# Performance work log

Hardware: AMD Instinct MI355X
Metric: run time of the kernel (lower is better)

The kernel has to match this reference:

```python
import jax, jax.numpy as jnp
import numpy as np

BETA = 0.25


def setup_inputs() -> dict:
    key = jax.random.key(0)
    k1, = jax.random.split(key, 1)
    N, D, LEVELS = 1048576, 32, 8
    z_e = jax.random.normal(k1, (N, D), dtype=jnp.float32)
    grid = jnp.linspace(-1.0, 1.0, LEVELS, dtype=jnp.float32)  # FSQ buffer
    return {"z_e": z_e, "grid": grid}


def reference(z_e, grid):
    levels = grid.shape[0]  # static
    z_norm = jnp.tanh(z_e)                                   # [N, D]
    # nearest-level search over the tiny grid (faithful abs-distance argmin)
    dist = jnp.abs(z_norm[:, :, None] - grid[None, None, :])  # [N, D, L]
    indices = jnp.argmin(dist, axis=-1)                       # [N, D] int
    z_q = grid[indices]                                       # [N, D]

    codebook_loss = jnp.mean((z_q - jax.lax.stop_gradient(z_norm)) ** 2)
    commitment_loss = jnp.mean((z_norm - jax.lax.stop_gradient(z_q)) ** 2)
    loss = codebook_loss + BETA * commitment_loss

    # straight-through estimator
    z_q_st = z_norm + jax.lax.stop_gradient(z_q - z_norm)

    # mixed code over first <=4 dims, perplexity = unique fraction
    code_dims = min(indices.shape[1], 4)
    bases = (levels ** jnp.arange(code_dims)).astype(indices.dtype)  # [code_dims]
    mixed_indices = jnp.sum(indices[:, :code_dims] * bases[None, :], axis=1)  # [N]
    n_codes = levels ** code_dims  # static small (4096)
    occupancy = jnp.bincount(mixed_indices, length=n_codes) > 0
    unique_codes = jnp.sum(occupancy).astype(z_e.dtype)
    perplexity = unique_codes / jnp.asarray(float(max(mixed_indices.size, 1)), z_e.dtype)

    return z_q_st, mixed_indices, loss, perplexity
```

## Files before the change

### kernel.cpp

```cpp
#include <hip/hip_runtime.h>
#include <math.h>

#define DD 32
#define NB 2048
#define BS 256

typedef float f32x4 __attribute__((ext_vector_type(4)));

__device__ __forceinline__ unsigned int fkey(float f) {
    unsigned int u = __float_as_uint(f);
    return (u & 0x80000000u) ? ~u : (u | 0x80000000u);
}
__device__ __forceinline__ float funkey(unsigned int k) {
    unsigned int u = (k & 0x80000000u) ? (k ^ 0x80000000u) : ~k;
    return __uint_as_float(u);
}

__global__ __launch_bounds__(256) void fsq_main(
    const float* __restrict__ ze,
    const float* __restrict__ grid,
    float* __restrict__ out,
    int N,
    float* __restrict__ partials,
    int* __restrict__ occ)
{
    __shared__ float gs[8];
    __shared__ float ts[7];
    if (threadIdx.x < 8) gs[threadIdx.x] = grid[threadIdx.x];
    if (threadIdx.x < 7) {
        float a = grid[threadIdx.x], b = grid[threadIdx.x + 1];
        unsigned int lo = fkey(a), hi = fkey(b);
        while (hi - lo > 1u) {
            unsigned int mid = lo + (hi - lo) / 2u;
            float x = funkey(mid);
            if (fabsf(x - b) < fabsf(x - a)) hi = mid; else lo = mid;
        }
        ts[threadIdx.x] = funkey(lo);
    }
    __syncthreads();

    const int Q = N * DD / 4;
    const int stride = gridDim.x * blockDim.x;
    float lsum = 0.f;

    auto body = [&](int i) {
        f32x4 w = __builtin_nontemporal_load((const f32x4*)ze + i);
        float xs[4] = {w.x, w.y, w.z, w.w};
        float tns[4];
        int bis[4];
        bool bad = false;
#pragma unroll
        for (int e = 0; e < 4; ++e) {
            float x = xs[e];
            float ex = __expf(2.0f * x);
            float r = __builtin_amdgcn_rcpf(ex + 1.0f);
            float tn = __builtin_fmaf(-2.0f, r, 1.0f);
            float u = __builtin_fmaf(tn, 3.5f, 3.5f);
            float ur = rintf(u);
            float fd = u - ur;
            bad = bad || (fabsf(fd) > 0.4999650f);
            float uc = fminf(7.0f, fmaxf(0.0f, ur));
            tns[e] = tn;
            bis[e] = (int)uc;
        }
        if (bad) {
#pragma unroll
            for (int e = 0; e < 4; ++e) {
                float tn = (float)tanh((double)xs[e]);
                int b = 0;
#pragma unroll
                for (int j = 0; j < 7; ++j) b += (tn > ts[j]) ? 1 : 0;
                tns[e] = tn;
                bis[e] = b;
            }
        }
        float os[4];
#pragma unroll
        for (int e = 0; e < 4; ++e) {
            float zq = gs[bis[e]];
            float d1 = zq - tns[e];
            lsum = __builtin_fmaf(d1, d1, lsum);
            os[e] = tns[e] + d1;
        }
        f32x4 ov = {os[0], os[1], os[2], os[3]};
        __builtin_nontemporal_store(ov, (f32x4*)out + i);

        if ((i & 7) == 0) {
            int mixed = bis[0] | (bis[1] << 3) | (bis[2] << 6) | (bis[3] << 9);
            __builtin_nontemporal_store((float)mixed,
                                        out + (size_t)N * DD + (i >> 3));
            occ[mixed] = 1;
        }
    };

    int i = blockIdx.x * blockDim.x + threadIdx.x;
    for (; i + stride < Q; i += 2 * stride) {
        body(i);
        body(i + stride);
    }
    if (i < Q) body(i);

    float s = lsum;
#pragma unroll
    for (int off = 32; off > 0; off >>= 1) s += __shfl_down(s, off);
    __shared__ float sh[4];
    if ((threadIdx.x & 63) == 0) sh[threadIdx.x >> 6] = s;
    __syncthreads();
    if (threadIdx.x == 0)
        partials[blockIdx.x] = sh[0] + sh[1] + sh[2] + sh[3];
}

__global__ __launch_bounds__(256) void fsq_tail(
    const float* __restrict__ partials, int nblocks,
    const int* __restrict__ occ,
    float* __restrict__ out, int N)
{
    double s = 0.0;
    for (int i = threadIdx.x; i < nblocks; i += 256) s += (double)partials[i];
    int cnt = 0;
    for (int i = threadIdx.x; i < 4096; i += 256) cnt += (occ[i] == 1) ? 1 : 0;
#pragma unroll
    for (int off = 32; off > 0; off >>= 1) {
        s += __shfl_down(s, off);
        cnt += __shfl_down(cnt, off);
    }
    __shared__ double shs[4];
    __shared__ int shc[4];
    if ((threadIdx.x & 63) == 0) { shs[threadIdx.x >> 6] = s; shc[threadIdx.x >> 6] = cnt; }
    __syncthreads();
    if (threadIdx.x == 0) {
        double total = shs[0] + shs[1] + shs[2] + shs[3];
        int unique = shc[0] + shc[1] + shc[2] + shc[3];
        double mean = total / ((double)N * (double)DD);
        size_t base = (size_t)N * DD + (size_t)N;
        out[base] = (float)(1.25 * mean);
        out[base + 1] = (float)unique / (float)N;
    }
}

extern "C" void kernel_launch(void* const* d_in, const int* in_sizes, int n_in,
                              void* d_out, int out_size, void* d_ws, size_t ws_size,
                              hipStream_t stream) {
    const float* ze   = (const float*)d_in[0];
    const float* grid = (const float*)d_in[1];
    float* out = (float*)d_out;
    int N = in_sizes[0] / DD;

    float* partials = (float*)d_ws;
    int* occ = (int*)((char*)d_ws + 8192);

    fsq_main<<<NB, BS, 0, stream>>>(ze, grid, out, N, partials, occ);
    fsq_tail<<<1, 256, 0, stream>>>(partials, NB, occ, out, N);
}
```

Measured before the change: 245.2 us.

## Software-pipeline loads, keep grid in registers, use regular stores

Restructures the grid-stride loop into a double-buffered software pipeline that prefetches the next pair of float4 inputs while the current pair is computed, so more loads are in flight per thread. The shared-memory grid lookup becomes a register select tree. Output stores change from nontemporal to ordinary stores. The fast path needs the stride to divide the work evenly, raises register pressure, and the changed store hint may affect cache behaviour.

```diff
diff --git a/kernel.cpp b/kernel.cpp
--- a/kernel.cpp
+++ b/kernel.cpp
@@ -24,9 +24,7 @@
     float* __restrict__ partials,
     int* __restrict__ occ)
 {
-    __shared__ float gs[8];
     __shared__ float ts[7];
-    if (threadIdx.x < 8) gs[threadIdx.x] = grid[threadIdx.x];
     if (threadIdx.x < 7) {
         float a = grid[threadIdx.x], b = grid[threadIdx.x + 1];
         unsigned int lo = fkey(a), hi = fkey(b);
@@ -37,14 +35,15 @@
         }
         ts[threadIdx.x] = funkey(lo);
     }
+    const float g0 = grid[0], g1 = grid[1], g2 = grid[2], g3 = grid[3],
+                g4 = grid[4], g5 = grid[5], g6 = grid[6], g7 = grid[7];
     __syncthreads();
 
     const int Q = N * DD / 4;
     const int stride = gridDim.x * blockDim.x;
     float lsum = 0.f;
 
-    auto body = [&](int i) {
-        f32x4 w = __builtin_nontemporal_load((const f32x4*)ze + i);
+    auto compute = [&](f32x4 w, f32x4 &ov, int &mix) {
         float xs[4] = {w.x, w.y, w.z, w.w};
         float tns[4];
         int bis[4];
@@ -77,28 +76,72 @@
         float os[4];
 #pragma unroll
         for (int e = 0; e < 4; ++e) {
-            float zq = gs[bis[e]];
+            int bi = bis[e];
+            float s01 = (bi & 1) ? g1 : g0;
+            float s23 = (bi & 1) ? g3 : g2;
+            float s45 = (bi & 1) ? g5 : g4;
+            float s67 = (bi & 1) ? g7 : g6;
+            float t03 = (bi & 2) ? s23 : s01;
+            float t47 = (bi & 2) ? s67 : s45;
+            float zq  = (bi & 4) ? t47 : t03;
             float d1 = zq - tns[e];
             lsum = __builtin_fmaf(d1, d1, lsum);
             os[e] = tns[e] + d1;
         }
-        f32x4 ov = {os[0], os[1], os[2], os[3]};
-        __builtin_nontemporal_store(ov, (f32x4*)out + i);
+        ov.x = os[0]; ov.y = os[1]; ov.z = os[2]; ov.w = os[3];
+        mix = bis[0] | (bis[1] << 3) | (bis[2] << 6) | (bis[3] << 9);
+    };
 
+    auto phase = [&](int i, f32x4 w0, f32x4 w1) {
+        f32x4 o0, o1; int m0, m1;
+        compute(w0, o0, m0);
+        compute(w1, o1, m1);
+        *((f32x4*)out + i) = o0;
+        *((f32x4*)out + i + stride) = o1;
         if ((i & 7) == 0) {
-            int mixed = bis[0] | (bis[1] << 3) | (bis[2] << 6) | (bis[3] << 9);
-            __builtin_nontemporal_store((float)mixed,
-                                        out + (size_t)N * DD + (i >> 3));
-            occ[mixed] = 1;
+            size_t mb = (size_t)N * DD;
+            out[mb + (i >> 3)] = (float)m0;
+            out[mb + ((i + stride) >> 3)] = (float)m1;
+            occ[m0] = 1;
+            occ[m1] = 1;
+        }
+    };
+
+    auto processOne = [&](int i, f32x4 w) {
+        f32x4 o; int m;
+        compute(w, o, m);
+        *((f32x4*)out + i) = o;
+        if ((i & 7) == 0) {
+            out[(size_t)N * DD + (i >> 3)] = (float)m;
+            occ[m] = 1;
         }
     };
 
     int i = blockIdx.x * blockDim.x + threadIdx.x;
-    for (; i + stride < Q; i += 2 * stride) {
-        body(i);
-        body(i + stride);
+    const bool fast = (stride % 8 == 0) && (Q % (4 * stride) == 0);
+    if (fast) {
+        const int T = Q / (2 * stride);
+        f32x4 a0 = __builtin_nontemporal_load((const f32x4*)ze + i);
+        f32x4 a1 = __builtin_nontemporal_load((const f32x4*)ze + i + stride);
+        for (int k = 0; k < T; k += 2) {
+            const int ib = i + 2 * stride;
+            f32x4 b0 = __builtin_nontemporal_load((const f32x4*)ze + ib);
+            f32x4 b1 = __builtin_nontemporal_load((const f32x4*)ze + ib + stride);
+            phase(i, a0, a1);
+            if (k + 2 < T) {
+                const int ia = ib + 2 * stride;
+                a0 = __builtin_nontemporal_load((const f32x4*)ze + ia);
+                a1 = __builtin_nontemporal_load((const f32x4*)ze + ia + stride);
+            }
+            phase(ib, b0, b1);
+            i = ib + 2 * stride;
+        }
+    } else {
+        for (; i < Q; i += stride) {
+            f32x4 w = __builtin_nontemporal_load((const f32x4*)ze + i);
+            processOne(i, w);
+        }
     }
-    if (i < Q) body(i);
 
     float s = lsum;
 #pragma unroll
```

Measured after the change: 246.2 us. About the same (+0.4%).

## Add fully unrolled fixed-trip kernel with load prefetch and register grid select

Applied to the files above, without the earlier changes.

Adds a specialized kernel that runs when the size exactly matches 16 iterations per thread. The loop is fully unrolled and loads are prefetched two iterations ahead to keep more memory requests in flight. The LDS grid lookup is replaced by a register select tree, and the mixed-index writes are deferred to the end of the loop. Output stores change from nontemporal to normal stores, which alters cache behaviour, and the extra prefetched registers may reduce occupancy.

```diff
diff --git a/kernel.cpp b/kernel.cpp
--- a/kernel.cpp
+++ b/kernel.cpp
@@ -4,6 +4,8 @@
 #define DD 32
 #define NB 2048
 #define BS 256
+#define STRIDE (NB * BS)
+#define TRIP 16
 
 typedef float f32x4 __attribute__((ext_vector_type(4)));
 
@@ -16,7 +18,84 @@
     return __uint_as_float(u);
 }
 
-__global__ __launch_bounds__(256) void fsq_main(
+
+#define FSQ_PREAMBLE                                                         \
+    __shared__ float ts[7];                                                  \
+    if (threadIdx.x < 7) {                                                   \
+        float a = grid[threadIdx.x], b = grid[threadIdx.x + 1];              \
+        unsigned int lo = fkey(a), hi = fkey(b);                             \
+        while (hi - lo > 1u) {                                               \
+            unsigned int mid = lo + (hi - lo) / 2u;                          \
+            float x = funkey(mid);                                           \
+            if (fabsf(x - b) < fabsf(x - a)) hi = mid; else lo = mid;        \
+        }                                                                    \
+        ts[threadIdx.x] = funkey(lo);                                        \
+    }                                                                        \
+    const float g0 = grid[0], g1 = grid[1], g2 = grid[2], g3 = grid[3],      \
+                g4 = grid[4], g5 = grid[5], g6 = grid[6], g7 = grid[7];      \
+    __syncthreads();
+
+#define FSQ_COMPUTE_LAMBDA                                                   \
+    auto compute = [&](f32x4 w, f32x4 &ov, int &mix) {                       \
+        float xs[4] = {w.x, w.y, w.z, w.w};                                  \
+        float tns[4];                                                        \
+        int bis[4];                                                          \
+        bool bad = false;                                                    \
+        _Pragma("unroll")                                                    \
+        for (int e = 0; e < 4; ++e) {                                        \
+            float x = xs[e];                                                 \
+            float ex = __expf(2.0f * x);                                     \
+            float r = __builtin_amdgcn_rcpf(ex + 1.0f);                      \
+            float tn = __builtin_fmaf(-2.0f, r, 1.0f);                       \
+            float u = __builtin_fmaf(tn, 3.5f, 3.5f);                        \
+            float ur = rintf(u);                                             \
+            float fd = u - ur;                                               \
+            bad = bad || (fabsf(fd) > 0.4999650f);                           \
+            float uc = fminf(7.0f, fmaxf(0.0f, ur));                         \
+            tns[e] = tn;                                                     \
+            bis[e] = (int)uc;                                                \
+        }                                                                    \
+        if (bad) {      \
+            _Pragma("unroll")                                                \
+            for (int e = 0; e < 4; ++e) {                                    \
+                float tn = (float)tanh((double)xs[e]);                       \
+                int b = 0;                                                   \
+                _Pragma("unroll")                                            \
+                for (int j = 0; j < 7; ++j) b += (tn > ts[j]) ? 1 : 0;       \
+                tns[e] = tn;                                                 \
+                bis[e] = b;                                                  \
+            }                                                                \
+        }                                                                    \
+        float os[4];                                                         \
+        _Pragma("unroll")                                                    \
+        for (int e = 0; e < 4; ++e) {                                        \
+            int bi = bis[e];                                                 \
+            float s01 = (bi & 1) ? g1 : g0;                                  \
+            float s23 = (bi & 1) ? g3 : g2;                                  \
+            float s45 = (bi & 1) ? g5 : g4;                                  \
+            float s67 = (bi & 1) ? g7 : g6;                                  \
+            float t03 = (bi & 2) ? s23 : s01;                                \
+            float t47 = (bi & 2) ? s67 : s45;                                \
+            float zq  = (bi & 4) ? t47 : t03;                                \
+            float d1 = zq - tns[e];                                          \
+            lsum = __builtin_fmaf(d1, d1, lsum);                             \
+            os[e] = tns[e] + d1;                                             \
+        }                                                                    \
+        ov.x = os[0]; ov.y = os[1]; ov.z = os[2]; ov.w = os[3];              \
+        mix = bis[0] | (bis[1] << 3) | (bis[2] << 6) | (bis[3] << 9);        \
+    };
+
+#define FSQ_LOSS_REDUCE                                                      \
+    float s = lsum;                                                          \
+    _Pragma("unroll")                                                        \
+    for (int off = 32; off > 0; off >>= 1) s += __shfl_down(s, off);         \
+    __shared__ float sh[4];                                                  \
+    if ((threadIdx.x & 63) == 0) sh[threadIdx.x >> 6] = s;                   \
+    __syncthreads();                                                         \
+    if (threadIdx.x == 0)                                                    \
+        partials[blockIdx.x] = sh[0] + sh[1] + sh[2] + sh[3];
+
+__global__ __launch_bounds__(256) void fsq_main_16(
     const float* __restrict__ ze,
     const float* __restrict__ grid,
     float* __restrict__ out,
@@ -24,90 +103,68 @@
     float* __restrict__ partials,
     int* __restrict__ occ)
 {
-    __shared__ float gs[8];
-    __shared__ float ts[7];
-    if (threadIdx.x < 8) gs[threadIdx.x] = grid[threadIdx.x];
-    if (threadIdx.x < 7) {
-        float a = grid[threadIdx.x], b = grid[threadIdx.x + 1];
-        unsigned int lo = fkey(a), hi = fkey(b);
-        while (hi - lo > 1u) {
-            unsigned int mid = lo + (hi - lo) / 2u;
-            float x = funkey(mid);
-            if (fabsf(x - b) < fabsf(x - a)) hi = mid; else lo = mid;
+    FSQ_PREAMBLE
+    float lsum = 0.f;
+    FSQ_COMPUTE_LAMBDA
+
+    const int tid = blockIdx.x * BS + threadIdx.x;
+    unsigned int pk[TRIP / 2] = {0, 0, 0, 0, 0, 0, 0, 0};
+    f32x4 w[TRIP];
+
+    w[0] = __builtin_nontemporal_load((const f32x4*)ze + tid);
+    w[1] = __builtin_nontemporal_load((const f32x4*)ze + tid + STRIDE);
+#pragma unroll
+    for (int k = 0; k < TRIP; ++k) {
+        if (k + 2 < TRIP)
+            w[k + 2] = __builtin_nontemporal_load(
+                (const f32x4*)ze + tid + (k + 2) * STRIDE);
+        f32x4 ov; int mix;
+        compute(w[k], ov, mix);
+        pk[k >> 1] |= (unsigned int)mix << ((k & 1) * 12);
+        *((f32x4*)out + tid + k * STRIDE) = ov;
+    }
+
+    if ((tid & 7) == 0) {
+        const size_t mb = (size_t)N * DD;
+        const int base = tid >> 3;
+#pragma unroll
+        for (int k = 0; k < TRIP; ++k) {
+            int m = (int)((pk[k >> 1] >> ((k & 1) * 12)) & 0xFFFu);
+            out[mb + base + k * (STRIDE / 8)] = (float)m;
+            occ[m] = 1;
         }
-        ts[threadIdx.x] = funkey(lo);
-    }
-    __syncthreads();
+    }
+
+    FSQ_LOSS_REDUCE
+}
+
+__global__ __launch_bounds__(256) void fsq_main_gen(
+    const float* __restrict__ ze,
+    const float* __restrict__ grid,
+    float* __restrict__ out,
+    int N,
+    float* __restrict__ partials,
+    int* __restrict__ occ)
+{
+    FSQ_PREAMBLE
+    float lsum = 0.f;
+    FSQ_COMPUTE_LAMBDA
 
     const int Q = N * DD / 4;
     const int stride = gridDim.x * blockDim.x;
-    float lsum = 0.f;
-
-    auto body = [&](int i) {
+    int i = blockIdx.x * blockDim.x + threadIdx.x;
+    for (; i < Q; i += stride) {
         f32x4 w = __builtin_nontemporal_load((const f32x4*)ze + i);
-        float xs[4] = {w.x, w.y, w.z, w.w};
-        float tns[4];
-        int bis[4];
-        bool bad = false;
-#pragma unroll
-        for (int e = 0; e < 4; ++e) {
-            float x = xs[e];
-            float ex = __expf(2.0f * x);
-            float r = __builtin_amdgcn_rcpf(ex + 1.0f);
-            float tn = __builtin_fmaf(-2.0f, r, 1.0f);
-            float u = __builtin_fmaf(tn, 3.5f, 3.5f);
-            float ur = rintf(u);
-            float fd = u - ur;
-            bad = bad || (fabsf(fd) > 0.4999650f);
-            float uc = fminf(7.0f, fmaxf(0.0f, ur));
-            tns[e] = tn;
-            bis[e] = (int)uc;
+        f32x4 o; int m;
+        compute(w, o, m);
+        *((f32x4*)out + i) = o;
+        if ((i & 7) == 0) {
+            out[(size_t)N * DD + (i >> 3)] = (float)m;
+            occ[m] = 1;
         }
-        if (bad) {
-#pragma unroll
-            for (int e = 0; e < 4; ++e) {
-                float tn = (float)tanh((double)xs[e]);
-                int b = 0;
-#pragma unroll
-                for (int j = 0; j < 7; ++j) b += (tn > ts[j]) ? 1 : 0;
-                tns[e] = tn;
-                bis[e] = b;
-            }
-        }
-        float os[4];
-#pragma unroll
-        for (int e = 0; e < 4; ++e) {
-            float zq = gs[bis[e]];
-            float d1 = zq - tns[e];
-            lsum = __builtin_fmaf(d1, d1, lsum);
-            os[e] = tns[e] + d1;
-        }
-        f32x4 ov = {os[0], os[1], os[2], os[3]};
-        __builtin_nontemporal_store(ov, (f32x4*)out + i);
-
-        if ((i & 7) == 0) {
-            int mixed = bis[0] | (bis[1] << 3) | (bis[2] << 6) | (bis[3] << 9);
-            __builtin_nontemporal_store((float)mixed,
-                                        out + (size_t)N * DD + (i >> 3));
-            occ[mixed] = 1;
-        }
-    };
-
-    int i = blockIdx.x * blockDim.x + threadIdx.x;
-    for (; i + stride < Q; i += 2 * stride) {
-        body(i);
-        body(i + stride);
-    }
-    if (i < Q) body(i);
-
-    float s = lsum;
-#pragma unroll
-    for (int off = 32; off > 0; off >>= 1) s += __shfl_down(s, off);
-    __shared__ float sh[4];
-    if ((threadIdx.x & 63) == 0) sh[threadIdx.x >> 6] = s;
-    __syncthreads();
-    if (threadIdx.x == 0)
-        partials[blockIdx.x] = sh[0] + sh[1] + sh[2] + sh[3];
+    }
+
+    FSQ_LOSS_REDUCE
 }
 
 __global__ __launch_bounds__(256) void fsq_tail(
@@ -149,6 +206,9 @@
     float* partials = (float*)d_ws;
     int* occ = (int*)((char*)d_ws + 8192);
 
-    fsq_main<<<NB, BS, 0, stream>>>(ze, grid, out, N, partials, occ);
+    if (N * (DD / 4) == TRIP * STRIDE)
+        fsq_main_16<<<NB, BS, 0, stream>>>(ze, grid, out, N, partials, occ);
+    else
+        fsq_main_gen<<<NB, BS, 0, stream>>>(ze, grid, out, N, partials, occ);
     fsq_tail<<<1, 256, 0, stream>>>(partials, NB, occ, out, N);
 }
```

Measured after the change: 248.2 us. No clear change (+1.2%).

## Launch one thread per vector instead of grid-stride loop, select grid levels in registers

Applied to the files above, without the earlier changes.

Replaces the fixed 2048-block grid-stride loop with one block per 256 float4 vectors (32768 blocks), so each thread handles a single element group. The shared-memory grid table is replaced by a register select tree over the eight grid values. Non-temporal loads stay, but output stores become ordinary stores. The tail kernel widens to 1024 threads to reduce the larger partials array. The many-block launch adds per-block setup (the bisection for thresholds, the barrier, the reduction) and many more partial sums in exchange for more parallelism and less loop overhead.

```diff
diff --git a/kernel.cpp b/kernel.cpp
--- a/kernel.cpp
+++ b/kernel.cpp
@@ -2,7 +2,6 @@
 #include <math.h>
 
 #define DD 32
-#define NB 2048
 #define BS 256
 
 typedef float f32x4 __attribute__((ext_vector_type(4)));
@@ -24,9 +23,7 @@
     float* __restrict__ partials,
     int* __restrict__ occ)
 {
-    __shared__ float gs[8];
     __shared__ float ts[7];
-    if (threadIdx.x < 8) gs[threadIdx.x] = grid[threadIdx.x];
     if (threadIdx.x < 7) {
         float a = grid[threadIdx.x], b = grid[threadIdx.x + 1];
         unsigned int lo = fkey(a), hi = fkey(b);
@@ -37,13 +34,15 @@
         }
         ts[threadIdx.x] = funkey(lo);
     }
+    const float g0 = grid[0], g1 = grid[1], g2 = grid[2], g3 = grid[3],
+                g4 = grid[4], g5 = grid[5], g6 = grid[6], g7 = grid[7];
     __syncthreads();
 
     const int Q = N * DD / 4;
-    const int stride = gridDim.x * blockDim.x;
+    const int i = blockIdx.x * BS + threadIdx.x;
     float lsum = 0.f;
 
-    auto body = [&](int i) {
+    if (i < Q) {
         f32x4 w = __builtin_nontemporal_load((const f32x4*)ze + i);
         float xs[4] = {w.x, w.y, w.z, w.w};
         float tns[4];
@@ -77,28 +76,27 @@
         float os[4];
 #pragma unroll
         for (int e = 0; e < 4; ++e) {
-            float zq = gs[bis[e]];
+            int bi = bis[e];
+            float s01 = (bi & 1) ? g1 : g0;
+            float s23 = (bi & 1) ? g3 : g2;
+            float s45 = (bi & 1) ? g5 : g4;
+            float s67 = (bi & 1) ? g7 : g6;
+            float t03 = (bi & 2) ? s23 : s01;
+            float t47 = (bi & 2) ? s67 : s45;
+            float zq  = (bi & 4) ? t47 : t03;
             float d1 = zq - tns[e];
             lsum = __builtin_fmaf(d1, d1, lsum);
             os[e] = tns[e] + d1;
         }
         f32x4 ov = {os[0], os[1], os[2], os[3]};
-        __builtin_nontemporal_store(ov, (f32x4*)out + i);
+        *((f32x4*)out + i) = ov;
 
         if ((i & 7) == 0) {
             int mixed = bis[0] | (bis[1] << 3) | (bis[2] << 6) | (bis[3] << 9);
-            __builtin_nontemporal_store((float)mixed,
-                                        out + (size_t)N * DD + (i >> 3));
+            out[(size_t)N * DD + (i >> 3)] = (float)mixed;
             occ[mixed] = 1;
         }
-    };
-
-    int i = blockIdx.x * blockDim.x + threadIdx.x;
-    for (; i + stride < Q; i += 2 * stride) {
-        body(i);
-        body(i + stride);
     }
-    if (i < Q) body(i);
 
     float s = lsum;
 #pragma unroll
@@ -110,27 +108,29 @@
         partials[blockIdx.x] = sh[0] + sh[1] + sh[2] + sh[3];
 }
 
-__global__ __launch_bounds__(256) void fsq_tail(
+__global__ __launch_bounds__(1024) void fsq_tail(
     const float* __restrict__ partials, int nblocks,
     const int* __restrict__ occ,
     float* __restrict__ out, int N)
 {
     double s = 0.0;
-    for (int i = threadIdx.x; i < nblocks; i += 256) s += (double)partials[i];
+    for (int i = threadIdx.x; i < nblocks; i += 1024) s += (double)partials[i];
     int cnt = 0;
-    for (int i = threadIdx.x; i < 4096; i += 256) cnt += (occ[i] == 1) ? 1 : 0;
+    for (int i = threadIdx.x; i < 4096; i += 1024) cnt += (occ[i] == 1) ? 1 : 0;
 #pragma unroll
     for (int off = 32; off > 0; off >>= 1) {
         s += __shfl_down(s, off);
         cnt += __shfl_down(cnt, off);
     }
-    __shared__ double shs[4];
-    __shared__ int shc[4];
+    __shared__ double shs[16];
+    __shared__ int shc[16];
     if ((threadIdx.x & 63) == 0) { shs[threadIdx.x >> 6] = s; shc[threadIdx.x >> 6] = cnt; }
     __syncthreads();
     if (threadIdx.x == 0) {
-        double total = shs[0] + shs[1] + shs[2] + shs[3];
-        int unique = shc[0] + shc[1] + shc[2] + shc[3];
+        double total = 0.0;
+        int unique = 0;
+#pragma unroll
+        for (int k = 0; k < 16; ++k) { total += shs[k]; unique += shc[k]; }
         double mean = total / ((double)N * (double)DD);
         size_t base = (size_t)N * DD + (size_t)N;
         out[base] = (float)(1.25 * mean);
@@ -146,9 +146,12 @@
     float* out = (float*)d_out;
     int N = in_sizes[0] / DD;
 
-    float* partials = (float*)d_ws;
-    int* occ = (int*)((char*)d_ws + 8192);
+    const int Q = N * (DD / 4);
+    const int nblocks = (Q + BS - 1) / BS;
 
-    fsq_main<<<NB, BS, 0, stream>>>(ze, grid, out, N, partials, occ);
-    fsq_tail<<<1, 256, 0, stream>>>(partials, NB, occ, out, N);
+    int* occ = (int*)d_ws;
+    float* partials = (float*)((char*)d_ws + 16384);
+
+    fsq_main<<<nblocks, BS, 0, stream>>>(ze, grid, out, N, partials, occ);
+    fsq_tail<<<1, 1024, 0, stream>>>(partials, nblocks, occ, out, N);
 }
```

New measurement: 275.1 us. 1.12x slower.
